# Kernel optimization log

Hardware: AMD Instinct MI355X
Metric: run time of the kernel (lower is better)

The kernel has to match this reference:

```python
import jax, jax.numpy as jnp
import numpy as np

H = 8          # num_heads
WIN = 256      # window_size (even); half-window = 128
NEG = -1e30    # stand-in for -inf that keeps softmax grad finite


def setup_inputs() -> dict:
    key = jax.random.key(0)
    ks = jax.random.split(key, 6)
    B, S, D, E = 2, 2048, 512, 512
    x = jax.random.normal(ks[0], (B, S, D), dtype=jnp.float32)
    padding_mask = jax.random.randint(ks[1], (B, S), 0, 2, dtype=jnp.int32)
    Wqkv = jax.random.normal(ks[2], (3 * E, D), dtype=jnp.float32) * 0.02
    bqkv = jnp.zeros((3 * E,), dtype=jnp.float32)
    Wo = jax.random.normal(ks[3], (E, E), dtype=jnp.float32) * 0.02
    bo = jnp.zeros((E,), dtype=jnp.float32)
    return {"x": x, "padding_mask": padding_mask, "Wqkv": Wqkv, "bqkv": bqkv,
            "Wo": Wo, "bo": bo}


def reference(x, padding_mask, Wqkv, bqkv, Wo, bo):
    B, S, _ = x.shape
    E = Wo.shape[0]
    Dh = E // H
    # qkv projection -> [B, H, S, 3*Dh]
    qkv = (x @ Wqkv.T + bqkv).reshape(B, S, H, 3 * Dh).transpose(0, 2, 1, 3)
    q, k, v = jnp.split(qkv, 3, axis=-1)
    # full S x S scores (original materializes [B,H,S,S]); scale by sqrt(head_dim)
    scores = jnp.einsum('bhsd,bhtd->bhst', q, k) / jnp.sqrt(jnp.float32(Dh))
    # sliding-window band: |i - j| <= window_size // 2
    i = jnp.arange(S)[:, None]
    j = jnp.arange(S)[None, :]
    band = jnp.abs(i - j) <= (WIN // 2)               # [S, S]
    # padding: entry valid only if both row and col tokens are non-pad
    pad = padding_mask.astype(bool)                    # [B, S]
    valid = band[None, None] & pad[:, None, None, :] & pad[:, None, :, None]
    scores = jnp.where(valid, scores, NEG)
    A = jax.nn.softmax(scores, axis=-1)
    # rows with no valid entry -> nan_to_num(., 0) in original -> zeros here
    row_valid = jnp.any(valid, axis=-1, keepdims=True)
    A = jnp.where(row_valid, A, 0.0)
    Y = jnp.einsum('bhst,bhtd->bhsd', A, v)            # [B,H,S,Dh]
    Y = Y.transpose(0, 2, 1, 3).reshape(B, S, E)
    return Y @ Wo.T + bo
```

## Files before the change

### kernel.cpp

```cpp
#include <hip/hip_runtime.h>

#define NH   8
#define SEQ  2048
#define DIM  512
#define EMB  512
#define DH   64
#define HALF 128
#define QT   16
#define KW   272
#define SCS  276

typedef __attribute__((ext_vector_type(8))) short short8;
typedef __attribute__((ext_vector_type(4))) float f32x4;

__device__ __forceinline__ unsigned short f2bf(float f) {
    unsigned int u = __float_as_uint(f);
    return (unsigned short)((u + 0x7fffu + ((u >> 16) & 1u)) >> 16);
}

__device__ __forceinline__ unsigned cvtpk(float lo, float hi) {
    unsigned r;
    asm("v_cvt_pk_bf16_f32 %0, %1, %2" : "=v"(r) : "v"(lo), "v"(hi));
    return r;
}

__device__ __forceinline__ void gload_lds16(const void* g, void* l) {
    __builtin_amdgcn_global_load_lds((__attribute__((address_space(1))) void*)g,
                                     (__attribute__((address_space(3))) void*)l,
                                     16, 0, 0);
}

__global__ __launch_bounds__(256)
void gemm_qkv(const float* __restrict__ A, const float* __restrict__ B,
              const float* __restrict__ bias, unsigned short* __restrict__ qkvh,
              unsigned short* __restrict__ vT) {
    constexpr int BM = 128, BN = 64, BK = 64;
    __shared__ unsigned short As[BM * BK];
    __shared__ unsigned short Bs[BN * BK];
    const int bid = blockIdx.x;
    const int wg = (bid & 7) * 96 + (bid >> 3);
    const int bm = (wg / 24) * BM, bn = (wg % 24) * BN;
    const int t = threadIdx.x, lane = t & 63, wid = t >> 6;
    const int wr = wid >> 1, wc = wid & 1;
    const int lr = lane & 15, lg = lane >> 4;

    f32x4 acc[4][2];
    #pragma unroll
    for (int m = 0; m < 4; ++m)
        #pragma unroll
        for (int n = 0; n < 2; ++n)
            acc[m][n] = (f32x4){0.f, 0.f, 0.f, 0.f};

    for (int kt = 0; kt < DIM; kt += BK) {
        #pragma unroll
        for (int i = 0; i < 4; ++i) {
            const int c = t + 256 * i, r = c >> 3, c8 = c & 7;
            const float4* src = (const float4*)(A + (size_t)(bm + r) * DIM + kt + c8 * 8);
            const float4 v0 = src[0], v1 = src[1];
            const uint4 pk = make_uint4(cvtpk(v0.x, v0.y), cvtpk(v0.z, v0.w),
                                        cvtpk(v1.x, v1.y), cvtpk(v1.z, v1.w));
            *(uint4*)&As[r * 64 + ((c8 ^ (r & 7)) << 3)] = pk;
        }
        #pragma unroll
        for (int i = 0; i < 2; ++i) {
            const int c = t + 256 * i, r = c >> 3, c8 = c & 7;
            const float4* src = (const float4*)(B + (size_t)(bn + r) * DIM + kt + c8 * 8);
            const float4 v0 = src[0], v1 = src[1];
            const uint4 pk = make_uint4(cvtpk(v0.x, v0.y), cvtpk(v0.z, v0.w),
                                        cvtpk(v1.x, v1.y), cvtpk(v1.z, v1.w));
            *(uint4*)&Bs[r * 64 + ((c8 ^ (r & 7)) << 3)] = pk;
        }
        __syncthreads();
        short8 af[2][4], bf[2][2];
        #pragma unroll
        for (int kk = 0; kk < 2; ++kk) {
            #pragma unroll
            for (int m = 0; m < 4; ++m) {
                const int row = wr * 64 + m * 16 + lr;
                af[kk][m] = *(const short8*)&As[row * 64 + (((kk * 4 + lg) ^ (row & 7)) << 3)];
            }
            #pragma unroll
            for (int n = 0; n < 2; ++n) {
                const int row = wc * 32 + n * 16 + lr;
                bf[kk][n] = *(const short8*)&Bs[row * 64 + (((kk * 4 + lg) ^ (row & 7)) << 3)];
            }
        }
        #pragma unroll
        for (int kk = 0; kk < 2; ++kk)
            #pragma unroll
            for (int m = 0; m < 4; ++m)
                #pragma unroll
                for (int n = 0; n < 2; ++n)
                    acc[m][n] = __builtin_amdgcn_mfma_f32_16x16x32_bf16(af[kk][m], bf[kk][n], acc[m][n], 0, 0, 0);
        __syncthreads();
    }

    unsigned short* Tr = As;
    #pragma unroll
    for (int n = 0; n < 2; ++n) {
        const int cl = wc * 32 + n * 16 + lr;
        const float bv = bias[bn + cl];
        #pragma unroll
        for (int m = 0; m < 4; ++m)
            #pragma unroll
            for (int r = 0; r < 4; ++r)
                Tr[(wr * 64 + m * 16 + lg * 4 + r) * 72 + cl] = f2bf(acc[m][n][r] + bv);
    }
    __syncthreads();

    const int h = bn / 192, ty = (bn >> 6) % 3;
    const int bb = bm >> 11, s0 = bm & 2047;
    if (ty < 2) {
        unsigned short* plane = qkvh + (((size_t)(bb * NH + h) * 3 + ty) * SEQ) * DH;
        const int s = t >> 1, hf = (t & 1) * 32;
        unsigned short* dst = plane + (size_t)(s0 + s) * DH + hf;
        #pragma unroll
        for (int k8 = 0; k8 < 4; ++k8)
            *(short8*)&dst[k8 * 8] = *(const short8*)&Tr[s * 72 + hf + k8 * 8];
    } else {
        const int d = t >> 2, pp = t & 3;
        unsigned short* vrow = vT + ((size_t)(bb * NH + h) * DH + d) * SEQ + s0 + pp * 32;
        #pragma unroll
        for (int k8 = 0; k8 < 4; ++k8) {
            alignas(16) unsigned short tmp[8];
            #pragma unroll
            for (int k = 0; k < 8; ++k) tmp[k] = Tr[(pp * 32 + k8 * 8 + k) * 72 + d];
            *(short8*)&vrow[k8 * 8] = *(short8*)tmp;
        }
    }
}

__global__ __launch_bounds__(256)
void attn_mfma(const unsigned short* __restrict__ qkvh,
               const unsigned short* __restrict__ vT,
               const int* __restrict__ pad,
               unsigned short* __restrict__ Yb) {
    const int bid = blockIdx.x;
    const int wg = (bid & 7) * 256 + (bid >> 3);
    const int bh = wg >> 7, qt = wg & 127;
    const int b = bh >> 3, h = bh & 7;
    const int i0 = qt * QT, kb = i0 - HALF;
    const int t = threadIdx.x, lane = t & 63, w = t >> 6;
    const int lr = lane & 15, lg = lane >> 4;

    __shared__ float Sc[QT * SCS];

    const unsigned short* Qg = qkvh + ((size_t)bh * 3 + 0) * SEQ * DH;
    const unsigned short* Kg = qkvh + ((size_t)bh * 3 + 1) * SEQ * DH;
    const unsigned short* vTg = vT + (size_t)bh * DH * SEQ;
    const int* padb = pad + b * SEQ;

    short8 qf[2];
    #pragma unroll
    for (int kk = 0; kk < 2; ++kk)
        qf[kk] = *(const short8*)&Qg[(size_t)(i0 + lr) * DH + kk * 32 + lg * 8];

    const int k0 = w * 16;
    #pragma unroll
    for (int c = 0; c < 5; ++c) {
        const int nc = (c < 4) ? 64 : 16;
        if (k0 < nc) {
            const int jl = c * 64 + k0 + lr;
            const int j = kb + jl;
            const int jc = j < 0 ? 0 : (j > SEQ - 1 ? SEQ - 1 : j);
            const int kv = (j >= 0 && j < SEQ) ? padb[j] : 0;
            f32x4 a0 = (f32x4){0.f, 0.f, 0.f, 0.f};
            __builtin_amdgcn_s_setprio(1);
            #pragma unroll
            for (int kk = 0; kk < 2; ++kk) {
                const short8 bfr = *(const short8*)&Kg[(size_t)jc * DH + kk * 32 + lg * 8];
                a0 = __builtin_amdgcn_mfma_f32_16x16x32_bf16(qf[kk], bfr, a0, 0, 0, 0);
            }
            __builtin_amdgcn_s_setprio(0);
            #pragma unroll
            for (int r = 0; r < 4; ++r) {
                const int q0 = lg * 4 + r;
                const bool ok = kv && (jl >= q0) && (jl <= q0 + 2 * HALF);
                Sc[q0 * SCS + jl] = ok ? a0[r] * 0.125f : -1e30f;
            }
        }
    }
    __syncthreads();

    for (int r = w; r < QT; r += 4) {
        float* row = &Sc[r * SCS];
        unsigned short* prow = (unsigned short*)row;
        if (!padb[i0 + r]) {
            #pragma unroll
            for (int u = 0; u < 5; ++u) {
                const int jl = lane + 64 * u;
                if (jl < KW) prow[jl] = 0;
            }
            if (lane >= 16 && lane < 32) prow[256 + lane] = 0;
            continue;
        }
        float v[5];
        float mx = -1e30f;
        #pragma unroll
        for (int u = 0; u < 5; ++u) {
            const int jl = lane + 64 * u;
            v[u] = (jl < KW) ? row[jl] : -1e30f;
            mx = fmaxf(mx, v[u]);
        }
        #pragma unroll
        for (int off = 32; off; off >>= 1) mx = fmaxf(mx, __shfl_xor(mx, off));
        float s = 0.f;
        #pragma unroll
        for (int u = 0; u < 5; ++u) { v[u] = __expf(v[u] - mx); s += v[u]; }
        #pragma unroll
        for (int off = 32; off; off >>= 1) s += __shfl_xor(s, off);
        const float inv = 1.f / s;
        asm volatile("" ::: "memory");
        #pragma unroll
        for (int u = 0; u < 5; ++u) {
            const int jl = lane + 64 * u;
            if (jl < KW) prow[jl] = f2bf(v[u] * inv);
        }
        if (lane >= 16 && lane < 32) prow[256 + lane] = 0;
    }
    __syncthreads();

    f32x4 o0 = (f32x4){0.f, 0.f, 0.f, 0.f};
    const unsigned short* PbU = (const unsigned short*)Sc;
    const int d0 = w * 16 + lr;
    #pragma unroll
    for (int c = 0; c < 5; ++c) {
        const int nkk = (c < 4) ? 2 : 1;
        #pragma unroll
        for (int kk = 0; kk < nkk; ++kk) {
            int j0 = kb + c * 64 + kk * 32 + lg * 8;
            j0 = j0 < 0 ? 0 : (j0 > SEQ - 8 ? SEQ - 8 : j0);
            const short8 vf = *(const short8*)&vTg[(size_t)d0 * SEQ + j0];
            const short8 pf = *(const short8*)&PbU[lr * (SCS * 2) + c * 64 + kk * 32 + lg * 8];
            __builtin_amdgcn_s_setprio(1);
            o0 = __builtin_amdgcn_mfma_f32_16x16x32_bf16(pf, vf, o0, 0, 0, 0);
            __builtin_amdgcn_s_setprio(0);
        }
    }

    #pragma unroll
    for (int r = 0; r < 4; ++r)
        Yb[(size_t)(b * SEQ + i0 + lg * 4 + r) * EMB + h * DH + d0] = f2bf(o0[r]);
}

__global__ __launch_bounds__(256)
void gemm_out(const unsigned short* __restrict__ A, const float* __restrict__ B,
              const float* __restrict__ bias, float* __restrict__ C) {
    constexpr int BM = 64, BN = 64, BK = 64;
    __shared__ unsigned short As[BM * BK];
    __shared__ unsigned short Bs[BN * BK];
    const int bid = blockIdx.x;
    const int wg = (bid & 7) * 64 + (bid >> 3);
    const int bm = (wg >> 3) * BM, bn = (wg & 7) * BN;
    const int t = threadIdx.x, lane = t & 63, wid = t >> 6;
    const int wr = wid >> 1, wc = wid & 1;
    const int lr = lane & 15, lg = lane >> 4;

    f32x4 acc[2][2];
    #pragma unroll
    for (int m = 0; m < 2; ++m)
        #pragma unroll
        for (int n = 0; n < 2; ++n)
            acc[m][n] = (f32x4){0.f, 0.f, 0.f, 0.f};

    for (int kt = 0; kt < DIM; kt += BK) {
        #pragma unroll
        for (int off = 0; off < BM * BK; off += 2048) {
            const int e = off + t * 8, r = e >> 6, c4 = (e & 63) >> 3;
            const int gc = (c4 ^ (r & 7)) << 3;
            gload_lds16(A + (size_t)(bm + r) * EMB + kt + gc, &As[e]);
        }
        #pragma unroll
        for (int i = 0; i < 2; ++i) {
            const int c = t + 256 * i, r = c >> 3, c8 = c & 7;
            const float4* src = (const float4*)(B + (size_t)(bn + r) * DIM + kt + c8 * 8);
            const float4 v0 = src[0], v1 = src[1];
            const uint4 pk = make_uint4(cvtpk(v0.x, v0.y), cvtpk(v0.z, v0.w),
                                        cvtpk(v1.x, v1.y), cvtpk(v1.z, v1.w));
            *(uint4*)&Bs[r * 64 + ((c8 ^ (r & 7)) << 3)] = pk;
        }
        __syncthreads();
        short8 af[2][2], bf[2][2];
        #pragma unroll
        for (int kk = 0; kk < 2; ++kk) {
            #pragma unroll
            for (int m = 0; m < 2; ++m) {
                const int row = wr * 32 + m * 16 + lr;
                af[kk][m] = *(const short8*)&As[row * BK + (((kk * 4 + lg) ^ (row & 7)) << 3)];
            }
            #pragma unroll
            for (int n = 0; n < 2; ++n) {
                const int row = wc * 32 + n * 16 + lr;
                bf[kk][n] = *(const short8*)&Bs[row * BK + (((kk * 4 + lg) ^ (row & 7)) << 3)];
            }
        }
        #pragma unroll
        for (int kk = 0; kk < 2; ++kk)
            #pragma unroll
            for (int m = 0; m < 2; ++m)
                #pragma unroll
                for (int n = 0; n < 2; ++n)
                    acc[m][n] = __builtin_amdgcn_mfma_f32_16x16x32_bf16(af[kk][m], bf[kk][n], acc[m][n], 0, 0, 0);
        __syncthreads();
    }

    const int orow = bm + wr * 32 + lg * 4;
    const int oc0 = bn + wc * 32 + lr;
    #pragma unroll
    for (int m = 0; m < 2; ++m)
        #pragma unroll
        for (int n = 0; n < 2; ++n) {
            const int col = oc0 + n * 16;
            const float bv = bias[col];
            #pragma unroll
            for (int r = 0; r < 4; ++r)
                C[(size_t)(orow + m * 16 + r) * EMB + col] = acc[m][n][r] + bv;
        }
}

extern "C" void kernel_launch(void* const* d_in, const int* in_sizes, int n_in,
                              void* d_out, int out_size, void* d_ws, size_t ws_size,
                              hipStream_t stream) {
    const float* x    = (const float*)d_in[0];
    const int*   pad  = (const int*)d_in[1];
    const float* Wqkv = (const float*)d_in[2];
    const float* bqkv = (const float*)d_in[3];
    const float* Wo   = (const float*)d_in[4];
    const float* bo   = (const float*)d_in[5];
    float* out = (float*)d_out;

    char* p = (char*)d_ws;
    unsigned short* qkvh = (unsigned short*)p;
    unsigned short* vT   = (unsigned short*)(p + 12582912);
    unsigned short* Yb   = (unsigned short*)(p + 16777216);

    dim3 blk(256);
    gemm_qkv<<<dim3(768), blk, 0, stream>>>(x, Wqkv, bqkv, qkvh, vT);
    attn_mfma<<<dim3(2048), blk, 0, stream>>>(qkvh, vT, pad, Yb);
    gemm_out<<<dim3(512), blk, 0, stream>>>(Yb, Wo, bo, out);
}
```

Baseline: 56.57 us.

## Process 32 query rows per attention block to reuse K and V fragments

Doubles the query tile per workgroup from 16 to 32 rows, so each K fragment and V fragment loaded from global memory feeds two MFMAs instead of one. The key window widens to 288 columns split into 18 tiles spread over the 4 waves, and the grid is halved to 1024 blocks. The aim is to cut redundant K/V global traffic across overlapping windows. In exchange the block needs more LDS, there are fewer blocks to spread across CUs, and each block computes more masked-out band columns.

After: 51.77 us. 1.09x faster.

```diff
diff --git a/kernel.cpp b/kernel.cpp
--- a/kernel.cpp
+++ b/kernel.cpp
@@ -6,9 +6,9 @@
 #define EMB  512
 #define DH   64
 #define HALF 128
-#define QT   16
-#define KW   272
-#define SCS  276
+#define QT   32
+#define KW2  288
+#define SCS2 292
 
 typedef __attribute__((ext_vector_type(8))) short short8;
 typedef __attribute__((ext_vector_type(4))) float f32x4;
@@ -136,62 +136,62 @@
                const int* __restrict__ pad,
                unsigned short* __restrict__ Yb) {
     const int bid = blockIdx.x;
-    const int wg = (bid & 7) * 256 + (bid >> 3);
-    const int bh = wg >> 7, qt = wg & 127;
+    const int wg = (bid & 7) * 128 + (bid >> 3);
+    const int bh = wg >> 6, qt = wg & 63;
     const int b = bh >> 3, h = bh & 7;
     const int i0 = qt * QT, kb = i0 - HALF;
     const int t = threadIdx.x, lane = t & 63, w = t >> 6;
     const int lr = lane & 15, lg = lane >> 4;
 
-    __shared__ float Sc[QT * SCS];
+    __shared__ float Sc[QT * SCS2];
 
     const unsigned short* Qg = qkvh + ((size_t)bh * 3 + 0) * SEQ * DH;
     const unsigned short* Kg = qkvh + ((size_t)bh * 3 + 1) * SEQ * DH;
     const unsigned short* vTg = vT + (size_t)bh * DH * SEQ;
     const int* padb = pad + b * SEQ;
 
-    short8 qf[2];
-    #pragma unroll
-    for (int kk = 0; kk < 2; ++kk)
-        qf[kk] = *(const short8*)&Qg[(size_t)(i0 + lr) * DH + kk * 32 + lg * 8];
-
-    const int k0 = w * 16;
-    #pragma unroll
-    for (int c = 0; c < 5; ++c) {
-        const int nc = (c < 4) ? 64 : 16;
-        if (k0 < nc) {
-            const int jl = c * 64 + k0 + lr;
-            const int j = kb + jl;
-            const int jc = j < 0 ? 0 : (j > SEQ - 1 ? SEQ - 1 : j);
-            const int kv = (j >= 0 && j < SEQ) ? padb[j] : 0;
-            f32x4 a0 = (f32x4){0.f, 0.f, 0.f, 0.f};
-            __builtin_amdgcn_s_setprio(1);
-            #pragma unroll
-            for (int kk = 0; kk < 2; ++kk) {
-                const short8 bfr = *(const short8*)&Kg[(size_t)jc * DH + kk * 32 + lg * 8];
-                a0 = __builtin_amdgcn_mfma_f32_16x16x32_bf16(qf[kk], bfr, a0, 0, 0, 0);
-            }
-            __builtin_amdgcn_s_setprio(0);
-            #pragma unroll
-            for (int r = 0; r < 4; ++r) {
-                const int q0 = lg * 4 + r;
-                const bool ok = kv && (jl >= q0) && (jl <= q0 + 2 * HALF);
-                Sc[q0 * SCS + jl] = ok ? a0[r] * 0.125f : -1e30f;
-            }
+    short8 qf[2][2];
+    #pragma unroll
+    for (int half = 0; half < 2; ++half)
+        #pragma unroll
+        for (int kk = 0; kk < 2; ++kk)
+            qf[half][kk] = *(const short8*)&Qg[(size_t)(i0 + half * 16 + lr) * DH + kk * 32 + lg * 8];
+
+    for (int tile = w; tile < 18; tile += 4) {
+        const int jl = tile * 16 + lr;
+        const int j = kb + jl;
+        const int jc = j < 0 ? 0 : (j > SEQ - 1 ? SEQ - 1 : j);
+        const int kv = (j >= 0 && j < SEQ) ? padb[j] : 0;
+        f32x4 a0 = (f32x4){0.f, 0.f, 0.f, 0.f};
+        f32x4 a1 = (f32x4){0.f, 0.f, 0.f, 0.f};
+        __builtin_amdgcn_s_setprio(1);
+        #pragma unroll
+        for (int kk = 0; kk < 2; ++kk) {
+            const short8 bfr = *(const short8*)&Kg[(size_t)jc * DH + kk * 32 + lg * 8];
+            a0 = __builtin_amdgcn_mfma_f32_16x16x32_bf16(qf[0][kk], bfr, a0, 0, 0, 0);
+            a1 = __builtin_amdgcn_mfma_f32_16x16x32_bf16(qf[1][kk], bfr, a1, 0, 0, 0);
+        }
+        __builtin_amdgcn_s_setprio(0);
+        #pragma unroll
+        for (int r = 0; r < 4; ++r) {
+            const int q0 = lg * 4 + r, q1 = 16 + q0;
+            const bool ok0 = kv && (jl >= q0) && (jl <= q0 + 2 * HALF);
+            const bool ok1 = kv && (jl >= q1) && (jl <= q1 + 2 * HALF);
+            Sc[q0 * SCS2 + jl] = ok0 ? a0[r] * 0.125f : -1e30f;
+            Sc[q1 * SCS2 + jl] = ok1 ? a1[r] * 0.125f : -1e30f;
         }
     }
     __syncthreads();
 
     for (int r = w; r < QT; r += 4) {
-        float* row = &Sc[r * SCS];
+        float* row = &Sc[r * SCS2];
         unsigned short* prow = (unsigned short*)row;
         if (!padb[i0 + r]) {
             #pragma unroll
             for (int u = 0; u < 5; ++u) {
                 const int jl = lane + 64 * u;
-                if (jl < KW) prow[jl] = 0;
-            }
-            if (lane >= 16 && lane < 32) prow[256 + lane] = 0;
+                if (jl < KW2) prow[jl] = 0;
+            }
             continue;
         }
         float v[5];
@@ -199,7 +199,7 @@
         #pragma unroll
         for (int u = 0; u < 5; ++u) {
             const int jl = lane + 64 * u;
-            v[u] = (jl < KW) ? row[jl] : -1e30f;
+            v[u] = (jl < KW2) ? row[jl] : -1e30f;
             mx = fmaxf(mx, v[u]);
         }
         #pragma unroll
@@ -214,33 +214,33 @@
         #pragma unroll
         for (int u = 0; u < 5; ++u) {
             const int jl = lane + 64 * u;
-            if (jl < KW) prow[jl] = f2bf(v[u] * inv);
-        }
-        if (lane >= 16 && lane < 32) prow[256 + lane] = 0;
+            if (jl < KW2) prow[jl] = f2bf(v[u] * inv);
+        }
     }
     __syncthreads();
 
     f32x4 o0 = (f32x4){0.f, 0.f, 0.f, 0.f};
+    f32x4 o1 = (f32x4){0.f, 0.f, 0.f, 0.f};
     const unsigned short* PbU = (const unsigned short*)Sc;
     const int d0 = w * 16 + lr;
     #pragma unroll
-    for (int c = 0; c < 5; ++c) {
-        const int nkk = (c < 4) ? 2 : 1;
-        #pragma unroll
-        for (int kk = 0; kk < nkk; ++kk) {
-            int j0 = kb + c * 64 + kk * 32 + lg * 8;
-            j0 = j0 < 0 ? 0 : (j0 > SEQ - 8 ? SEQ - 8 : j0);
-            const short8 vf = *(const short8*)&vTg[(size_t)d0 * SEQ + j0];
-            const short8 pf = *(const short8*)&PbU[lr * (SCS * 2) + c * 64 + kk * 32 + lg * 8];
-            __builtin_amdgcn_s_setprio(1);
-            o0 = __builtin_amdgcn_mfma_f32_16x16x32_bf16(pf, vf, o0, 0, 0, 0);
-            __builtin_amdgcn_s_setprio(0);
-        }
-    }
-
-    #pragma unroll
-    for (int r = 0; r < 4; ++r)
-        Yb[(size_t)(b * SEQ + i0 + lg * 4 + r) * EMB + h * DH + d0] = f2bf(o0[r]);
+    for (int c = 0; c < 9; ++c) {
+        int j0 = kb + c * 32 + lg * 8;
+        j0 = j0 < 0 ? 0 : (j0 > SEQ - 8 ? SEQ - 8 : j0);
+        const short8 vf  = *(const short8*)&vTg[(size_t)d0 * SEQ + j0];
+        const short8 pf0 = *(const short8*)&PbU[lr * (SCS2 * 2) + c * 32 + lg * 8];
+        const short8 pf1 = *(const short8*)&PbU[(16 + lr) * (SCS2 * 2) + c * 32 + lg * 8];
+        __builtin_amdgcn_s_setprio(1);
+        o0 = __builtin_amdgcn_mfma_f32_16x16x32_bf16(pf0, vf, o0, 0, 0, 0);
+        o1 = __builtin_amdgcn_mfma_f32_16x16x32_bf16(pf1, vf, o1, 0, 0, 0);
+        __builtin_amdgcn_s_setprio(0);
+    }
+
+    #pragma unroll
+    for (int r = 0; r < 4; ++r) {
+        Yb[(size_t)(b * SEQ + i0 + lg * 4 + r) * EMB + h * DH + d0]      = f2bf(o0[r]);
+        Yb[(size_t)(b * SEQ + i0 + 16 + lg * 4 + r) * EMB + h * DH + d0] = f2bf(o1[r]);
+    }
 }
 
 __global__ __launch_bounds__(256)
@@ -336,6 +336,6 @@
 
     dim3 blk(256);
     gemm_qkv<<<dim3(768), blk, 0, stream>>>(x, Wqkv, bqkv, qkvh, vT);
-    attn_mfma<<<dim3(2048), blk, 0, stream>>>(qkvh, vT, pad, Yb);
+    attn_mfma<<<dim3(1024), blk, 0, stream>>>(qkvh, vT, pad, Yb);
     gemm_out<<<dim3(512), blk, 0, stream>>>(Yb, Wo, bo, out);
 }
```
